# Kernel tuning notes

Measured on AMD Instinct MI355X. Metric: run time of the kernel, lower is better.

The kernel has to match this reference:

```python
import jax, jax.numpy as jnp
import numpy as np

D_K = 64.0  # key size from init


def setup_inputs() -> dict:
    key = jax.random.key(0)
    k1, k2, k3, k4, k5 = jax.random.split(key, 5)
    B, H, S, D = 2, 16, 2048, 64
    q = jax.random.normal(k1, (B, H, S, D), dtype=jnp.float32)
    v = jax.random.normal(k2, (B, H, S, D), dtype=jnp.float32)
    k = jax.random.normal(k3, (B, H, S, D), dtype=jnp.float32)
    att_mask = jax.random.normal(k4, (B, 1, S, S), dtype=jnp.float32)
    seq_mask = jax.random.uniform(k5, (B, 1, 1, S), dtype=jnp.float32)
    return {"q": q, "v": v, "k": k, "att_mask": att_mask, "seq_mask": seq_mask}


def reference(q, v, k, att_mask, seq_mask):
    # scores: [B, H, S, S]
    scores = jnp.einsum("bhqd,bhkd->bhqk", q, k) / jnp.sqrt(jnp.asarray(D_K, q.dtype))
    scores = scores + att_mask
    weights = jax.nn.softmax(scores, axis=-1)
    weights = weights * seq_mask  # post-softmax mask, no renormalization
    out = jnp.einsum("bhqk,bhkd->bhqd", weights, v)
    return out
```

## Files before the change

kernel.cpp:

```cpp
#include <hip/hip_runtime.h>
#include <hip/hip_bf16.h>
#include <stdint.h>

typedef __attribute__((ext_vector_type(8)))  short    short8;
typedef __attribute__((ext_vector_type(4)))  float    floatx4;
typedef __attribute__((ext_vector_type(16))) float    floatx16;
typedef __attribute__((ext_vector_type(2)))  uint32_t uintx2;

static __device__ __forceinline__ uint32_t cvtpk(float lo, float hi) {
  uint32_t r;
  asm("v_cvt_pk_bf16_f32 %0, %1, %2" : "=v"(r) : "v"(lo), "v"(hi));
  return r;
}

static __device__ __forceinline__ short8 pack8c(floatx4 a, floatx4 b) {
  union { uint32_t u[4]; short8 s; } r;
  r.u[0] = cvtpk(a[0], a[1]); r.u[1] = cvtpk(a[2], a[3]);
  r.u[2] = cvtpk(b[0], b[1]); r.u[3] = cvtpk(b[2], b[3]);
  return r.s;
}

#define MFMA32(a, b, c) __builtin_amdgcn_mfma_f32_32x32x16_bf16((a), (b), (c), 0, 0, 0)

#define TILE_BARRIER() asm volatile("s_waitcnt lgkmcnt(0)\n\ts_barrier" ::: "memory")

constexpr int S_LEN = 2048;
constexpr int DH    = 64;
constexpr int QBLK  = 128;
constexpr int KVBLK = 64;
constexpr int NT    = S_LEN / KVBLK;

static __device__ __forceinline__ void swap32(uint32_t& a, uint32_t& b, int hi) {
#if __has_builtin(__builtin_amdgcn_permlane32_swap)
  typedef int intx2 __attribute__((ext_vector_type(2)));
  intx2 r = __builtin_amdgcn_permlane32_swap((int)a, (int)b, false, false);
  a = (uint32_t)r[0]; b = (uint32_t)r[1];
#else
  uint32_t pa = (uint32_t)__shfl_xor((int)a, 32, 64);
  uint32_t pb = (uint32_t)__shfl_xor((int)b, 32, 64);
  uint32_t na = hi ? pb : a;
  uint32_t nb = hi ? b  : pa;
  a = na; b = nb;
#endif
}

__global__ __launch_bounds__(256, 2)
void attn_fwd(const float* __restrict__ Q, const float* __restrict__ V,
              const float* __restrict__ K, const float* __restrict__ AM,
              const float* __restrict__ SM, float* __restrict__ O)
{
  __shared__ ushort Kl[2][KVBLK * DH];
  __shared__ ushort Vt[2][DH * KVBLK];

  const int bh   = blockIdx.x;
  const int qt   = blockIdx.y;

  const int tid  = threadIdx.x;
  const int lane = tid & 63;
  const int wave = tid >> 6;
  const int l31  = lane & 31;
  const int hi   = lane >> 5;

  const float* qptr  = Q  + (size_t)bh * S_LEN * DH;
  const float* kptr  = K  + (size_t)bh * S_LEN * DH;
  const float* vptr  = V  + (size_t)bh * S_LEN * DH;
  const float* amptr = AM + (size_t)(bh >> 4) * S_LEN * S_LEN;
  const float* smptr = SM + (size_t)(bh >> 4) * S_LEN;
  float* optr = O + (size_t)bh * S_LEN * DH;

  const int qw = qt * QBLK + wave * 32;

  short8 qf[4];
  {
    const float* p = qptr + (size_t)(qw + l31) * DH + hi * 8;
    #pragma unroll
    for (int s = 0; s < 4; ++s) {
      floatx4 f0 = *(const floatx4*)(p + s * 16);
      floatx4 f1 = *(const floatx4*)(p + s * 16 + 4);
      qf[s] = pack8c(f0, f1);
    }
  }

  const int krow = tid >> 2;
  const int kcol = (tid & 3) * 16;
  const int kcb  = (tid & 3) * 2;
  const int vr0  = (tid & 15) * 4;
  const int vd0  = (tid >> 4) * 4;

  floatx4 kregA[4], vregA[4], kregB[4], vregB[4];
  floatx4 amx[2][4];

  auto LOADKV = [&](int t, floatx4 (&kreg)[4], floatx4 (&vreg)[4]) {
    const float* kg = kptr + (size_t)(t * KVBLK + krow) * DH + kcol;
    #pragma unroll
    for (int j = 0; j < 4; ++j) kreg[j] = ((const floatx4*)kg)[j];
    #pragma unroll
    for (int i = 0; i < 4; ++i)
      vreg[i] = *(const floatx4*)(vptr + (size_t)(t * KVBLK + vr0 + i) * DH + vd0);
  };

  auto WRITEKV = [&](int c, floatx4 (&kreg)[4], floatx4 (&vreg)[4]) {
    const int sw = krow & 7;
    *(short8*)&Kl[c][krow * 64 + ((kcb ^ sw) * 8)]       = pack8c(kreg[0], kreg[1]);
    *(short8*)&Kl[c][krow * 64 + (((kcb + 1) ^ sw) * 8)] = pack8c(kreg[2], kreg[3]);
    #pragma unroll
    for (int d = 0; d < 4; ++d) {
      uintx2 w;
      w[0] = cvtpk(vreg[0][d], vreg[1][d]);
      w[1] = cvtpk(vreg[2][d], vreg[3][d]);
      const int row = vd0 + d;
      const int ch  = (vr0 >> 3) ^ (row & 7);
      *(uintx2*)&Vt[c][row * 64 + ch * 8 + (vr0 & 7)] = w;
    }
  };

  auto LOADAM = [&](int t) {
    const float* base = amptr + (size_t)(qw + l31) * S_LEN + t * KVBLK + hi * 4;
    #pragma unroll
    for (int blk = 0; blk < 2; ++blk)
      #pragma unroll
      for (int j = 0; j < 4; ++j)
        amx[blk][j] = *(const floatx4*)(base + blk * 32 + j * 8);
  };

  LOADKV(0, kregA, vregA);
  WRITEKV(0, kregA, vregA);
  LOADKV(1, kregB, vregB);
  LOADAM(0);
  TILE_BARRIER();

  float m_run = -3.0e38f, l_run = 0.f;
  floatx16 oacc[2];
  #pragma unroll
  for (int db = 0; db < 2; ++db)
    #pragma unroll
    for (int r = 0; r < 16; ++r) oacc[db][r] = 0.f;

  auto STEP = [&](int tt, int c,
                  floatx4 (&kW)[4], floatx4 (&vW)[4],
                  floatx4 (&kL)[4], floatx4 (&vL)[4]) {
    floatx16 sc[2];
    __builtin_amdgcn_s_setprio(1);
    #pragma unroll
    for (int blk = 0; blk < 2; ++blk) {
      #pragma unroll
      for (int r = 0; r < 16; ++r) sc[blk][r] = 0.f;
      const int row = blk * 32 + l31;
      const int sw  = row & 7;
      #pragma unroll
      for (int s = 0; s < 4; ++s) {
        const int ch = (s * 2 + hi) ^ sw;
        short8 kf = *(const short8*)&Kl[c][row * 64 + ch * 8];
        sc[blk] = MFMA32(kf, qf[s], sc[blk]);
      }
    }
    __builtin_amdgcn_s_setprio(0);

    float pmax = -3.0e38f;
    #pragma unroll
    for (int blk = 0; blk < 2; ++blk)
      #pragma unroll
      for (int r = 0; r < 16; ++r) {
        const float v = fmaf(sc[blk][r], 0.125f, amx[blk][r >> 2][r & 3]);
        sc[blk][r] = v;
        pmax = fmaxf(pmax, v);
      }
    pmax = fmaxf(pmax, __shfl_xor(pmax, 32, 64));

    const int tn = (tt + 1 < NT) ? tt + 1 : NT - 1;
    LOADAM(tn);

    floatx4 smv[2][4];
    #pragma unroll
    for (int blk = 0; blk < 2; ++blk)
      #pragma unroll
      for (int j = 0; j < 4; ++j)
        smv[blk][j] = *(const floatx4*)(smptr + tt * KVBLK + blk * 32 + hi * 4 + j * 8);

    if (__any(pmax > m_run)) {
      const float mnew = fmaxf(m_run, pmax);
      const float fac  = __expf(m_run - mnew);
      float fw[16];
      #pragma unroll
      for (int r = 0; r < 16; ++r)
        fw[r] = __shfl(fac, (r & 3) + 8 * (r >> 2) + 4 * hi, 64);
      #pragma unroll
      for (int db = 0; db < 2; ++db)
        #pragma unroll
        for (int r = 0; r < 16; ++r) oacc[db][r] *= fw[r];
      l_run *= fac;
      m_run = mnew;
    }

    float ssum = 0.f;
    #pragma unroll
    for (int blk = 0; blk < 2; ++blk)
      #pragma unroll
      for (int r = 0; r < 16; ++r) {
        const float e = __expf(sc[blk][r] - m_run);
        sc[blk][r] = e;
        ssum += e;
      }
    ssum += __shfl_xor(ssum, 32, 64);
    l_run += ssum;

    uint32_t pw[2][2][4];
    #pragma unroll
    for (int blk = 0; blk < 2; ++blk)
      #pragma unroll
      for (int ks = 0; ks < 2; ++ks) {
        uint32_t w0 = cvtpk(sc[blk][ks * 8 + 0] * smv[blk][ks * 2 + 0][0],
                            sc[blk][ks * 8 + 1] * smv[blk][ks * 2 + 0][1]);
        uint32_t w1 = cvtpk(sc[blk][ks * 8 + 2] * smv[blk][ks * 2 + 0][2],
                            sc[blk][ks * 8 + 3] * smv[blk][ks * 2 + 0][3]);
        uint32_t w2 = cvtpk(sc[blk][ks * 8 + 4] * smv[blk][ks * 2 + 1][0],
                            sc[blk][ks * 8 + 5] * smv[blk][ks * 2 + 1][1]);
        uint32_t w3 = cvtpk(sc[blk][ks * 8 + 6] * smv[blk][ks * 2 + 1][2],
                            sc[blk][ks * 8 + 7] * smv[blk][ks * 2 + 1][3]);
        swap32(w0, w2, hi);
        swap32(w1, w3, hi);
        pw[blk][ks][0] = w0; pw[blk][ks][1] = w1;
        pw[blk][ks][2] = w2; pw[blk][ks][3] = w3;
      }

    __builtin_amdgcn_s_setprio(1);
    #pragma unroll
    for (int blk = 0; blk < 2; ++blk)
      #pragma unroll
      for (int ks = 0; ks < 2; ++ks) {
        union { uint32_t u[4]; short8 s; } af;
        af.u[0] = pw[blk][ks][0]; af.u[1] = pw[blk][ks][1];
        af.u[2] = pw[blk][ks][2]; af.u[3] = pw[blk][ks][3];
        #pragma unroll
        for (int db = 0; db < 2; ++db) {
          const int row = db * 32 + l31;
          const int ch  = (blk * 4 + ks * 2 + hi) ^ (row & 7);
          short8 vf = *(const short8*)&Vt[c][row * 64 + ch * 8];
          oacc[db] = MFMA32(af.s, vf, oacc[db]);
        }
      }
    __builtin_amdgcn_s_setprio(0);

    WRITEKV(c ^ 1, kW, vW);
    const int t2 = (tt + 2 < NT) ? tt + 2 : NT - 1;
    LOADKV(t2, kL, vL);
    TILE_BARRIER();
  };

  #pragma unroll 1
  for (int t = 0; t < NT; t += 2) {
    STEP(t,     0, kregB, vregB, kregA, vregA);
    STEP(t + 1, 1, kregA, vregA, kregB, vregB);
  }

  const float inv = 1.0f / l_run;
  float iw[16];
  #pragma unroll
  for (int r = 0; r < 16; ++r)
    iw[r] = __shfl(inv, (r & 3) + 8 * (r >> 2) + 4 * hi, 64);
  #pragma unroll
  for (int db = 0; db < 2; ++db)
    #pragma unroll
    for (int r = 0; r < 16; ++r) {
      const int qr = (r & 3) + 8 * (r >> 2) + 4 * hi;
      optr[(size_t)(qw + qr) * DH + db * 32 + l31] = oacc[db][r] * iw[r];
    }
}

extern "C" void kernel_launch(void* const* d_in, const int* in_sizes, int n_in,
                              void* d_out, int out_size, void* d_ws, size_t ws_size,
                              hipStream_t stream) {
  const float* q  = (const float*)d_in[0];
  const float* v  = (const float*)d_in[1];
  const float* k  = (const float*)d_in[2];
  const float* am = (const float*)d_in[3];
  const float* sm = (const float*)d_in[4];
  float* o = (float*)d_out;

  dim3 grid(32, S_LEN / QBLK);
  attn_fwd<<<grid, 256, 0, stream>>>(q, v, k, am, sm, o);
}
```

Before: 143.4 us.

## Stage attention-mask tiles through LDS with coalesced loads; shorten K/V prefetch

The att_mask tile is now read with row-contiguous, coalesced 16-byte global loads into registers. It is written into a padded per-wave LDS buffer and read back in the MFMA accumulator layout, replacing the earlier strided per-lane global reads. The K/V register double buffer drops to a single set that prefetches only one tile ahead, and that load is issued right after the QK MFMAs. This cuts register pressure and scattered mask traffic, but adds LDS use (about 34KB more), which may threaten 2 blocks/CU occupancy, and it leaves less time to hide K/V load latency.

```diff
diff --git a/kernel.cpp b/kernel.cpp
--- a/kernel.cpp
+++ b/kernel.cpp
@@ -29,6 +29,7 @@
 constexpr int QBLK  = 128;
 constexpr int KVBLK = 64;
 constexpr int NT    = S_LEN / KVBLK;
+constexpr int AMP   = 68;
 
 static __device__ __forceinline__ void swap32(uint32_t& a, uint32_t& b, int hi) {
 #if __has_builtin(__builtin_amdgcn_permlane32_swap)
@@ -51,6 +52,7 @@
 {
   __shared__ ushort Kl[2][KVBLK * DH];
   __shared__ ushort Vt[2][DH * KVBLK];
+  __shared__ float  am_lds[QBLK * AMP];
 
   const int bh   = blockIdx.x;
   const int qt   = blockIdx.y;
@@ -86,11 +88,14 @@
   const int kcb  = (tid & 3) * 2;
   const int vr0  = (tid & 15) * 4;
   const int vd0  = (tid >> 4) * 4;
-
-  floatx4 kregA[4], vregA[4], kregB[4], vregB[4];
-  floatx4 amx[2][4];
-
-  auto LOADKV = [&](int t, floatx4 (&kreg)[4], floatx4 (&vreg)[4]) {
+  const int arow = lane >> 4;
+  const int acol = (lane & 15) * 4;
+
+  floatx4 kreg[4], vreg[4];
+  floatx4 amstg[8];
+  float* amw = &am_lds[(wave * 32) * AMP];
+
+  auto LOADKV = [&](int t) {
     const float* kg = kptr + (size_t)(t * KVBLK + krow) * DH + kcol;
     #pragma unroll
     for (int j = 0; j < 4; ++j) kreg[j] = ((const floatx4*)kg)[j];
@@ -99,7 +104,7 @@
       vreg[i] = *(const floatx4*)(vptr + (size_t)(t * KVBLK + vr0 + i) * DH + vd0);
   };
 
-  auto WRITEKV = [&](int c, floatx4 (&kreg)[4], floatx4 (&vreg)[4]) {
+  auto WRITEKV = [&](int c) {
     const int sw = krow & 7;
     *(short8*)&Kl[c][krow * 64 + ((kcb ^ sw) * 8)]       = pack8c(kreg[0], kreg[1]);
     *(short8*)&Kl[c][krow * 64 + (((kcb + 1) ^ sw) * 8)] = pack8c(kreg[2], kreg[3]);
@@ -114,19 +119,23 @@
     }
   };
 
-  auto LOADAM = [&](int t) {
-    const float* base = amptr + (size_t)(qw + l31) * S_LEN + t * KVBLK + hi * 4;
-    #pragma unroll
-    for (int blk = 0; blk < 2; ++blk)
-      #pragma unroll
-      for (int j = 0; j < 4; ++j)
-        amx[blk][j] = *(const floatx4*)(base + blk * 32 + j * 8);
-  };
-
-  LOADKV(0, kregA, vregA);
-  WRITEKV(0, kregA, vregA);
-  LOADKV(1, kregB, vregB);
-  LOADAM(0);
+  auto LOADAM_G = [&](int t) {
+    #pragma unroll
+    for (int i = 0; i < 8; ++i)
+      amstg[i] = *(const floatx4*)(amptr + (size_t)(qw + i * 4 + arow) * S_LEN
+                                   + t * KVBLK + acol);
+  };
+
+  auto WRITEAM = [&]() {
+    #pragma unroll
+    for (int i = 0; i < 8; ++i)
+      *(floatx4*)&amw[(i * 4 + arow) * AMP + acol] = amstg[i];
+  };
+
+  LOADKV(0);
+  WRITEKV(0);
+  LOADAM_G(0);
+  WRITEAM();
   TILE_BARRIER();
 
   float m_run = -3.0e38f, l_run = 0.f;
@@ -136,9 +145,7 @@
     #pragma unroll
     for (int r = 0; r < 16; ++r) oacc[db][r] = 0.f;
 
-  auto STEP = [&](int tt, int c,
-                  floatx4 (&kW)[4], floatx4 (&vW)[4],
-                  floatx4 (&kL)[4], floatx4 (&vL)[4]) {
+  auto STEP = [&](int tt, int c) {
     floatx16 sc[2];
     __builtin_amdgcn_s_setprio(1);
     #pragma unroll
@@ -156,6 +163,20 @@
     }
     __builtin_amdgcn_s_setprio(0);
 
+    const int tn = (tt + 1 < NT) ? tt + 1 : NT - 1;
+    LOADKV(tn);
+    LOADAM_G(tn);
+
+    floatx4 amx[2][4];
+    {
+      const float* amr = &amw[l31 * AMP];
+      #pragma unroll
+      for (int blk = 0; blk < 2; ++blk)
+        #pragma unroll
+        for (int j = 0; j < 4; ++j)
+          amx[blk][j] = *(const floatx4*)&amr[blk * 32 + hi * 4 + j * 8];
+    }
+
     float pmax = -3.0e38f;
     #pragma unroll
     for (int blk = 0; blk < 2; ++blk)
@@ -166,9 +187,6 @@
         pmax = fmaxf(pmax, v);
       }
     pmax = fmaxf(pmax, __shfl_xor(pmax, 32, 64));
-
-    const int tn = (tt + 1 < NT) ? tt + 1 : NT - 1;
-    LOADAM(tn);
 
     floatx4 smv[2][4];
     #pragma unroll
@@ -241,16 +259,15 @@
       }
     __builtin_amdgcn_s_setprio(0);
 
-    WRITEKV(c ^ 1, kW, vW);
-    const int t2 = (tt + 2 < NT) ? tt + 2 : NT - 1;
-    LOADKV(t2, kL, vL);
+    WRITEKV(c ^ 1);
+    WRITEAM();
     TILE_BARRIER();
   };
 
   #pragma unroll 1
   for (int t = 0; t < NT; t += 2) {
-    STEP(t,     0, kregB, vregB, kregA, vregA);
-    STEP(t + 1, 1, kregA, vregA, kregB, vregB);
+    STEP(t,     0);
+    STEP(t + 1, 1);
   }
 
   const float inv = 1.0f / l_run;
```

New measurement: 143.6 us. About the same (+0.1%).

## Switch to single-wave blocks with per-wave K/V staging and no barriers

Applied to the files above, without the earlier changes.

Each block now runs one 64-lane wave handling 32 query rows, with single-buffered K and transposed-V tiles in LDS. Each wave loads and converts its own K/V tiles, prefetching the next tile into registers in halves interleaved with the softmax work. This removes block-wide barriers and the shared double buffer, and gives a grid four times larger. In exchange, K/V reuse across the four waves of a block is lost, so global K/V reads and bf16 conversion work grow fourfold per query.

```diff
diff --git a/kernel.cpp b/kernel.cpp
--- a/kernel.cpp
+++ b/kernel.cpp
@@ -13,20 +13,11 @@
   return r;
 }
 
-static __device__ __forceinline__ short8 pack8c(floatx4 a, floatx4 b) {
-  union { uint32_t u[4]; short8 s; } r;
-  r.u[0] = cvtpk(a[0], a[1]); r.u[1] = cvtpk(a[2], a[3]);
-  r.u[2] = cvtpk(b[0], b[1]); r.u[3] = cvtpk(b[2], b[3]);
-  return r.s;
-}
-
 #define MFMA32(a, b, c) __builtin_amdgcn_mfma_f32_32x32x16_bf16((a), (b), (c), 0, 0, 0)
-
-#define TILE_BARRIER() asm volatile("s_waitcnt lgkmcnt(0)\n\ts_barrier" ::: "memory")
 
 constexpr int S_LEN = 2048;
 constexpr int DH    = 64;
-constexpr int QBLK  = 128;
+constexpr int QBLK  = 32;
 constexpr int KVBLK = 64;
 constexpr int NT    = S_LEN / KVBLK;
 
@@ -44,20 +35,17 @@
 #endif
 }
 
-__global__ __launch_bounds__(256, 2)
+__global__ __launch_bounds__(64, 2)
 void attn_fwd(const float* __restrict__ Q, const float* __restrict__ V,
               const float* __restrict__ K, const float* __restrict__ AM,
               const float* __restrict__ SM, float* __restrict__ O)
 {
-  __shared__ ushort Kl[2][KVBLK * DH];
-  __shared__ ushort Vt[2][DH * KVBLK];
+  __shared__ ushort Kl[KVBLK * DH];
+  __shared__ ushort Vt[DH * KVBLK];
 
   const int bh   = blockIdx.x;
   const int qt   = blockIdx.y;
-
-  const int tid  = threadIdx.x;
-  const int lane = tid & 63;
-  const int wave = tid >> 6;
+  const int lane = threadIdx.x;
   const int l31  = lane & 31;
   const int hi   = lane >> 5;
 
@@ -68,7 +56,7 @@
   const float* smptr = SM + (size_t)(bh >> 4) * S_LEN;
   float* optr = O + (size_t)bh * S_LEN * DH;
 
-  const int qw = qt * QBLK + wave * 32;
+  const int qw = qt * QBLK;
 
   short8 qf[4];
   {
@@ -77,43 +65,56 @@
     for (int s = 0; s < 4; ++s) {
       floatx4 f0 = *(const floatx4*)(p + s * 16);
       floatx4 f1 = *(const floatx4*)(p + s * 16 + 4);
-      qf[s] = pack8c(f0, f1);
+      union { uint32_t u[4]; short8 v; } w;
+      w.u[0] = cvtpk(f0[0], f0[1]); w.u[1] = cvtpk(f0[2], f0[3]);
+      w.u[2] = cvtpk(f1[0], f1[1]); w.u[3] = cvtpk(f1[2], f1[3]);
+      qf[s] = w.v;
     }
   }
 
-  const int krow = tid >> 2;
-  const int kcol = (tid & 3) * 16;
-  const int kcb  = (tid & 3) * 2;
-  const int vr0  = (tid & 15) * 4;
-  const int vd0  = (tid >> 4) * 4;
-
-  floatx4 kregA[4], vregA[4], kregB[4], vregB[4];
+  const int ksw = lane & 7;
+  const int vr0 = (lane & 15) * 4;
+  const int vd0 = (lane >> 4) * 16;
+
+  floatx4 stgA[8], stgB[8];
   floatx4 amx[2][4];
 
-  auto LOADKV = [&](int t, floatx4 (&kreg)[4], floatx4 (&vreg)[4]) {
-    const float* kg = kptr + (size_t)(t * KVBLK + krow) * DH + kcol;
-    #pragma unroll
-    for (int j = 0; j < 4; ++j) kreg[j] = ((const floatx4*)kg)[j];
-    #pragma unroll
-    for (int i = 0; i < 4; ++i)
-      vreg[i] = *(const floatx4*)(vptr + (size_t)(t * KVBLK + vr0 + i) * DH + vd0);
-  };
-
-  auto WRITEKV = [&](int c, floatx4 (&kreg)[4], floatx4 (&vreg)[4]) {
-    const int sw = krow & 7;
-    *(short8*)&Kl[c][krow * 64 + ((kcb ^ sw) * 8)]       = pack8c(kreg[0], kreg[1]);
-    *(short8*)&Kl[c][krow * 64 + (((kcb + 1) ^ sw) * 8)] = pack8c(kreg[2], kreg[3]);
-    #pragma unroll
-    for (int d = 0; d < 4; ++d) {
+  auto LOADK = [&](int t, int h, floatx4 (&s)[8]) {
+    const float* g = kptr + (size_t)(t * KVBLK + lane) * DH + h * 32;
+    #pragma unroll
+    for (int j = 0; j < 8; ++j) s[j] = ((const floatx4*)g)[j];
+  };
+  auto WRITEK = [&](int h, floatx4 (&s)[8]) {
+    #pragma unroll
+    for (int j = 0; j < 4; ++j) {
+      union { uint32_t u[4]; short8 v; } w;
+      w.u[0] = cvtpk(s[2 * j][0], s[2 * j][1]);
+      w.u[1] = cvtpk(s[2 * j][2], s[2 * j][3]);
+      w.u[2] = cvtpk(s[2 * j + 1][0], s[2 * j + 1][1]);
+      w.u[3] = cvtpk(s[2 * j + 1][2], s[2 * j + 1][3]);
+      *(short8*)&Kl[lane * 64 + (((h * 4 + j) ^ ksw) * 8)] = w.v;
+    }
+  };
+  auto LOADV = [&](int t, int h, floatx4 (&s)[8]) {
+    #pragma unroll
+    for (int r = 0; r < 4; ++r) {
+      const float* g = vptr + (size_t)(t * KVBLK + vr0 + r) * DH + vd0 + h * 8;
+      s[r * 2]     = ((const floatx4*)g)[0];
+      s[r * 2 + 1] = ((const floatx4*)g)[1];
+    }
+  };
+  auto WRITEV = [&](int h, floatx4 (&s)[8]) {
+    #pragma unroll
+    for (int dd = 0; dd < 8; ++dd) {
+      const int d  = vd0 + h * 8 + dd;
+      const int q4 = dd >> 2, r4 = dd & 3;
       uintx2 w;
-      w[0] = cvtpk(vreg[0][d], vreg[1][d]);
-      w[1] = cvtpk(vreg[2][d], vreg[3][d]);
-      const int row = vd0 + d;
-      const int ch  = (vr0 >> 3) ^ (row & 7);
-      *(uintx2*)&Vt[c][row * 64 + ch * 8 + (vr0 & 7)] = w;
-    }
-  };
-
+      w[0] = cvtpk(s[0 + q4][r4], s[2 + q4][r4]);
+      w[1] = cvtpk(s[4 + q4][r4], s[6 + q4][r4]);
+      const int ch = (vr0 >> 3) ^ (d & 7);
+      *(uintx2*)&Vt[d * 64 + ch * 8 + (vr0 & 7)] = w;
+    }
+  };
   auto LOADAM = [&](int t) {
     const float* base = amptr + (size_t)(qw + l31) * S_LEN + t * KVBLK + hi * 4;
     #pragma unroll
@@ -123,11 +124,11 @@
         amx[blk][j] = *(const floatx4*)(base + blk * 32 + j * 8);
   };
 
-  LOADKV(0, kregA, vregA);
-  WRITEKV(0, kregA, vregA);
-  LOADKV(1, kregB, vregB);
+  LOADK(0, 0, stgA); LOADK(0, 1, stgB);
+  WRITEK(0, stgA);   WRITEK(1, stgB);
+  LOADV(0, 0, stgA); LOADV(0, 1, stgB);
+  WRITEV(0, stgA);   WRITEV(1, stgB);
   LOADAM(0);
-  TILE_BARRIER();
 
   float m_run = -3.0e38f, l_run = 0.f;
   floatx16 oacc[2];
@@ -136,9 +137,10 @@
     #pragma unroll
     for (int r = 0; r < 16; ++r) oacc[db][r] = 0.f;
 
-  auto STEP = [&](int tt, int c,
-                  floatx4 (&kW)[4], floatx4 (&vW)[4],
-                  floatx4 (&kL)[4], floatx4 (&vL)[4]) {
+  #pragma unroll 1
+  for (int t = 0; t < NT; ++t) {
+    const int tn = (t + 1 < NT) ? t + 1 : NT - 1;
+
     floatx16 sc[2];
     __builtin_amdgcn_s_setprio(1);
     #pragma unroll
@@ -149,12 +151,13 @@
       const int sw  = row & 7;
       #pragma unroll
       for (int s = 0; s < 4; ++s) {
-        const int ch = (s * 2 + hi) ^ sw;
-        short8 kf = *(const short8*)&Kl[c][row * 64 + ch * 8];
+        short8 kf = *(const short8*)&Kl[row * 64 + ((s * 2 + hi) ^ sw) * 8];
         sc[blk] = MFMA32(kf, qf[s], sc[blk]);
       }
     }
     __builtin_amdgcn_s_setprio(0);
+
+    LOADK(tn, 0, stgA);
 
     float pmax = -3.0e38f;
     #pragma unroll
@@ -167,15 +170,8 @@
       }
     pmax = fmaxf(pmax, __shfl_xor(pmax, 32, 64));
 
-    const int tn = (tt + 1 < NT) ? tt + 1 : NT - 1;
     LOADAM(tn);
-
-    floatx4 smv[2][4];
-    #pragma unroll
-    for (int blk = 0; blk < 2; ++blk)
-      #pragma unroll
-      for (int j = 0; j < 4; ++j)
-        smv[blk][j] = *(const floatx4*)(smptr + tt * KVBLK + blk * 32 + hi * 4 + j * 8);
+    LOADK(tn, 1, stgB);
 
     if (__any(pmax > m_run)) {
       const float mnew = fmaxf(m_run, pmax);
@@ -192,6 +188,8 @@
       m_run = mnew;
     }
 
+    WRITEK(0, stgA);
+
     float ssum = 0.f;
     #pragma unroll
     for (int blk = 0; blk < 2; ++blk)
@@ -203,6 +201,18 @@
       }
     ssum += __shfl_xor(ssum, 32, 64);
     l_run += ssum;
+
+    WRITEK(1, stgB);
+    LOADV(tn, 0, stgA);
+
+    floatx4 smv[2][4];
+    #pragma unroll
+    for (int blk = 0; blk < 2; ++blk)
+      #pragma unroll
+      for (int j = 0; j < 4; ++j)
+        smv[blk][j] = *(const floatx4*)(smptr + t * KVBLK + blk * 32 + hi * 4 + j * 8);
+
+    LOADV(tn, 1, stgB);
 
     uint32_t pw[2][2][4];
     #pragma unroll
@@ -235,22 +245,14 @@
         for (int db = 0; db < 2; ++db) {
           const int row = db * 32 + l31;
           const int ch  = (blk * 4 + ks * 2 + hi) ^ (row & 7);
-          short8 vf = *(const short8*)&Vt[c][row * 64 + ch * 8];
+          short8 vf = *(const short8*)&Vt[row * 64 + ch * 8];
           oacc[db] = MFMA32(af.s, vf, oacc[db]);
         }
       }
     __builtin_amdgcn_s_setprio(0);
 
-    WRITEKV(c ^ 1, kW, vW);
-    const int t2 = (tt + 2 < NT) ? tt + 2 : NT - 1;
-    LOADKV(t2, kL, vL);
-    TILE_BARRIER();
-  };
-
-  #pragma unroll 1
-  for (int t = 0; t < NT; t += 2) {
-    STEP(t,     0, kregB, vregB, kregA, vregA);
-    STEP(t + 1, 1, kregA, vregA, kregB, vregB);
+    WRITEV(0, stgA);
+    WRITEV(1, stgB);
   }
 
   const float inv = 1.0f / l_run;
@@ -278,5 +280,5 @@
   float* o = (float*)d_out;
 
   dim3 grid(32, S_LEN / QBLK);
-  attn_fwd<<<grid, 256, 0, stream>>>(q, v, k, am, sm, o);
-}
+  attn_fwd<<<grid, 64, 0, stream>>>(q, v, k, am, sm, o);
+}
```

Result: slower. 320.7 us (+123.6%).
